# Performance work log

Measured on AMD Instinct MI355X. Metric: run time of the kernel, lower is better.

Reference implementation:

```python
import jax, jax.numpy as jnp
import numpy as np

G = 64          # voxel grid side
N_IN = 150000   # input points
N_OUT = 150000  # output points
K = 3           # cubic kernel size
CIN = 32
FOUT = 64


def _make_cloud(rng, n):
    flat = rng.permutation(G ** 3)[:n]
    x = flat % G
    y = (flat // G) % G
    z = flat // (G * G)
    pos = np.stack([x, y, z], axis=-1).astype(np.float32) + 0.5  # voxel centers
    return flat, pos


def setup_inputs() -> dict:
    rng = np.random.default_rng(0)
    flat_in, inp_pos = _make_cloud(rng, N_IN)
    _, out_pos = _make_cloud(np.random.default_rng(1), N_OUT)

    # Fixed-radius (Linf, r = K*voxel*0.51 = 1.53) search on the grid ==
    # 3x3x3 voxel neighborhood lookup. Build dense voxel -> point-index map.
    grid = np.full(G ** 3, -1, dtype=np.int64)
    grid[flat_in] = np.arange(N_IN)
    offs = np.stack(np.meshgrid(*([np.arange(-1, 2)] * 3), indexing='ij'), -1).reshape(-1, 3)  # [27,3]
    out_vox = (out_pos - 0.5).astype(np.int64)              # [M,3]
    nb = out_vox[:, None, :] + offs[None, :, :]             # [M,27,3]
    inb = ((nb >= 0) & (nb < G)).all(-1)                    # [M,27]
    flat = nb[..., 0] + G * nb[..., 1] + G * G * nb[..., 2]
    flat = np.where(inb, flat, 0)
    found = grid[flat]
    mask = inb & (found >= 0)
    nbr_idx = np.where(mask, found, 0).astype(np.int32)

    key = jax.random.key(0)
    k1, k2, k3, k4, k5 = jax.random.split(key, 5)
    return {
        'inp_features': jax.random.normal(k1, (N_IN, CIN), jnp.float32),
        'inp_positions': jnp.asarray(inp_pos),
        'out_positions': jnp.asarray(out_pos),
        'voxel_size': jnp.asarray(1.0, jnp.float32),
        'inp_importance': jax.random.uniform(k2, (N_IN,), jnp.float32),
        'kernel': jax.random.uniform(k3, (K, K, K, CIN, FOUT), jnp.float32, -0.05, 0.05),
        'bias': jnp.zeros((FOUT,), jnp.float32) + 0.01 * jax.random.normal(k4, (FOUT,)),
        'neighbor_index': jnp.asarray(nbr_idx),
        'neighbor_mask': jnp.asarray(mask),
    }


def _sparse_conv(inp_features, inp_positions, out_positions, voxel_size,
                 inp_importance, kernel, bias, neighbor_index, neighbor_mask):
    # offset = 0 (odd kernel). extent = kernel_size * voxel_size.
    extent = K * voxel_size
    nbr_pos = inp_positions[neighbor_index]                  # [M,Kn,3]
    rel = nbr_pos - out_positions[:, None, :]                # [M,Kn,3]
    # identity coordinate mapping: normalize to [-1,1] over the extent
    n = 2.0 * rel / extent
    # align_corners=False mapping to filter coords, + offset (=0)
    fcoord = (n * 0.5 + 0.5) * K - 0.5                        # [M,Kn,3] (x,y,z)
    idx = jnp.clip(jnp.round(fcoord).astype(jnp.int32), 0, K - 1)
    # kernel is indexed [z,y,x,cin,cout]; positions are [x,y,z]
    flat_cell = idx[..., 2] * (K * K) + idx[..., 1] * K + idx[..., 0]   # [M,Kn]
    onehot = jax.nn.one_hot(flat_cell, K ** 3, dtype=inp_features.dtype)  # [M,Kn,27]
    w = (inp_importance[neighbor_index] * neighbor_mask.astype(inp_features.dtype))  # [M,Kn]
    feat = inp_features[neighbor_index] * w[..., None]       # [M,Kn,Cin]
    # accumulate neighbor features into their kernel cell, then contract with kernel
    cellfeat = jnp.einsum('mko,mkc->moc', onehot, feat)      # [M,27,Cin]
    wflat = kernel.reshape(K ** 3, CIN, FOUT)
    out = jnp.einsum('moc,ocf->mf', cellfeat, wflat)         # [M,F]
    return out + bias


def reference(inp_features, inp_positions, out_positions, voxel_size,
              inp_importance, kernel, bias, neighbor_index, neighbor_mask):
    return _sparse_conv(inp_features, inp_positions, out_positions, voxel_size,
                        inp_importance, kernel, bias, neighbor_index, neighbor_mask)
```

## Files before the change

### kernel.cpp

```cpp
#include <hip/hip_runtime.h>
#include <hip/hip_bf16.h>

#define CELLS 27
#define CIN   32
#define FOUT  64
#define M_OUT 150000
#define N_INP 150000
#define GDIM  64
#define NVOX  (GDIM * GDIM * GDIM)

#define GFEAT_SHORTS (NVOX * CIN)
#define GFEAT_BYTES  (GFEAT_SHORTS * 2)
#define OUTMAP_BYTES (NVOX * 4)
#define WT2_SHORTS   (CELLS * 4 * 64 * 8)
#define WT2_BYTES    (WT2_SHORTS * 2)
#define DENSE_WS     ((size_t)GFEAT_BYTES + OUTMAP_BYTES + WT2_BYTES)

#define ZROW  N_INP
#define PPG   64
#define GROUPS ((M_OUT + PPG - 1) / PPG)
#define FB_ROWS  (N_INP + 1)
#define FB_BYTES (FB_ROWS * CIN * 2)

typedef __attribute__((ext_vector_type(4))) float f32x4;
typedef __attribute__((ext_vector_type(8))) short bf16x8;
typedef __attribute__((ext_vector_type(4))) int   i32x4;

__device__ __forceinline__ short f2bf(float x) {
    union { __hip_bfloat16 h; short s; } u;
    u.h = __float2bfloat16(x);
    return u.s;
}


__global__ __launch_bounds__(256) void clear_kernel(unsigned short* __restrict__ gfeat,
                                                    int* __restrict__ outmap) {
    int t = blockIdx.x * 256 + threadIdx.x;
    if (t < 1048576) {
        ((i32x4*)gfeat)[t] = (i32x4){0, 0, 0, 0};
    } else {
        int u = t - 1048576;
        if (u < 65536) ((i32x4*)outmap)[u] = (i32x4){-1, -1, -1, -1};
    }
}

__global__ __launch_bounds__(256) void build_kernel(const float* __restrict__ feat,
                                                    const float* __restrict__ ipos,
                                                    const float* __restrict__ opos,
                                                    const float* __restrict__ imp,
                                                    const float* __restrict__ W,
                                                    unsigned short* __restrict__ gfeat,
                                                    int* __restrict__ outmap,
                                                    unsigned short* __restrict__ Wt2) {
    int t = blockIdx.x * 256 + threadIdx.x;
    if (t < N_INP * 4) {
        int p = t >> 2, c = t & 3;
        int x = (int)ipos[p * 3 + 0];
        int y = (int)ipos[p * 3 + 1];
        int z = (int)ipos[p * 3 + 2];
        int flat = x + (y << 6) + (z << 12);
        float wv = imp[p];
        const float* fp = feat + (size_t)p * CIN + c * 8;
        f32x4 f0 = *(const f32x4*)fp;
        f32x4 f1 = *(const f32x4*)(fp + 4);
        bf16x8 o;
        o[0] = f2bf(f0.x * wv); o[1] = f2bf(f0.y * wv);
        o[2] = f2bf(f0.z * wv); o[3] = f2bf(f0.w * wv);
        o[4] = f2bf(f1.x * wv); o[5] = f2bf(f1.y * wv);
        o[6] = f2bf(f1.z * wv); o[7] = f2bf(f1.w * wv);
        *(bf16x8*)(gfeat + (size_t)flat * CIN + c * 8) = o;
    } else if (t < N_INP * 4 + M_OUT) {
        int m = t - N_INP * 4;
        int x = (int)opos[m * 3 + 0];
        int y = (int)opos[m * 3 + 1];
        int z = (int)opos[m * 3 + 2];
        outmap[x + (y << 6) + (z << 12)] = m;
    } else {
        int v = t - (N_INP * 4 + M_OUT);
        if (v < CELLS * 4 * 64) {
            int l    = v & 63;
            int ct   = v >> 6;
            int tt   = ct & 3;
            int cell = ct >> 2;
            int fout = tt * 16 + (l & 15);
            int cin0 = (l >> 4) * 8;
            bf16x8 o;
#pragma unroll
            for (int j = 0; j < 8; ++j)
                o[j] = f2bf(W[cell * 2048 + (cin0 + j) * 64 + fout]);
            *(bf16x8*)(Wt2 + (size_t)v * 8) = o;
        }
    }
}

__global__ __launch_bounds__(256, 2) void conv_dense_kernel(
        const unsigned short* __restrict__ gfeat,
        const int*   __restrict__ outmap,
        const unsigned short* __restrict__ Wt2,
        const float* __restrict__ bias,
        float* __restrict__ out) {
    __shared__ __align__(16) unsigned char sh[48000];

    const int tid = threadIdx.x;
    const int bid = blockIdx.x;
    const int bx0 = (bid & 7) * 8;
    const int by0 = ((bid >> 3) & 7) * 8;
    const int bz0 = (bid >> 6) * 4;

#pragma unroll
    for (int it = 0; it < 10; ++it) {
        int c = it * 256 + tid;
        if (c < 2400) {
            int v = c >> 2, ch = c & 3;
            int q10  = (v * 6554) >> 16;
            int hx   = v - q10 * 10;
            int q100 = (q10 * 6554) >> 16;
            int hy   = q10 - q100 * 10;
            int hz   = q100;
            int gx = bx0 - 1 + hx, gy = by0 - 1 + hy, gz = bz0 - 1 + hz;
            bf16x8 val = {0, 0, 0, 0, 0, 0, 0, 0};
            if (((unsigned)gx < 64u) & ((unsigned)gy < 64u) & ((unsigned)gz < 64u)) {
                int flat = gx + (gy << 6) + (gz << 12);
                val = *(const bf16x8*)(gfeat + (size_t)flat * CIN + ch * 8);
            }
            *(bf16x8*)&sh[v * 80 + ch * 16] = val;
        }
    }
    __syncthreads();

    const int w    = tid >> 6;
    const int lane = tid & 63;
    const int r = lane & 15;
    const int g = lane >> 4;

    const unsigned char* Ab = sh + (r & 7) * 80 + (r >> 3) * 800 + w * 8000 + g * 16;
    const unsigned short* Bp = Wt2 + lane * 8;

    f32x4 acc[4][4];
#pragma unroll
    for (int mt = 0; mt < 4; ++mt)
#pragma unroll
        for (int nt = 0; nt < 4; ++nt) acc[mt][nt] = (f32x4){0.f, 0.f, 0.f, 0.f};

    bf16x8 bb[2][4];
#pragma unroll
    for (int nt = 0; nt < 4; ++nt)
        bb[0][nt] = *(const bf16x8*)(Bp + nt * 512);

#pragma unroll
    for (int cell = 0; cell < CELLS; ++cell) {
        const int cur = cell & 1, nxt = cur ^ 1;
        const int hx = cell % 3, hy = (cell / 3) % 3, hz = cell / 9;
        if (cell + 1 < CELLS) {
#pragma unroll
            for (int nt = 0; nt < 4; ++nt)
                bb[nxt][nt] = *(const bf16x8*)(Bp + (cell + 1) * 2048 + nt * 512);
        }
#pragma unroll
        for (int mt = 0; mt < 4; ++mt) {
            bf16x8 a = *(const bf16x8*)(Ab + hz * 8000 + (hy + 2 * mt) * 800 + hx * 80);
#pragma unroll
            for (int nt = 0; nt < 4; ++nt)
                acc[mt][nt] = __builtin_amdgcn_mfma_f32_16x16x32_bf16(a, bb[cur][nt],
                                                                      acc[mt][nt], 0, 0, 0);
        }
    }

    float bv0 = bias[r], bv1 = bias[16 + r], bv2 = bias[32 + r], bv3 = bias[48 + r];
    const int obase = bx0 + (by0 << 6) + ((bz0 + w) << 12);
#pragma unroll
    for (int mt = 0; mt < 4; ++mt) {
#pragma unroll
        for (int j = 0; j < 4; ++j) {
            int row = mt * 16 + g * 4 + j;
            int om = outmap[obase + (row & 7) + ((row >> 3) << 6)];
            if (om >= 0) {
                float* op = out + (size_t)om * FOUT + r;
                op[0]  = acc[mt][0][j] + bv0;
                op[16] = acc[mt][1][j] + bv1;
                op[32] = acc[mt][2][j] + bv2;
                op[48] = acc[mt][3][j] + bv3;
            }
        }
    }
}


#define CELL_OF(k) (((k) % 3) * 9 + (((k) / 3) % 3) * 3 + ((k) / 9))

__global__ __launch_bounds__(256) void prep_fb_kernel(const float* __restrict__ W,
                                                      const float* __restrict__ feat,
                                                      const float* __restrict__ imp,
                                                      unsigned short* __restrict__ Wt2,
                                                      unsigned short* __restrict__ fb) {
    int t = blockIdx.x * 256 + threadIdx.x;
    if (t < FB_ROWS * 4) {
        int i = t >> 2, c = t & 3;
        bf16x8 o = {0, 0, 0, 0, 0, 0, 0, 0};
        if (i < N_INP) {
            float w = imp[i];
            const float* fp = feat + (size_t)i * CIN + c * 8;
            f32x4 f0 = *(const f32x4*)fp;
            f32x4 f1 = *(const f32x4*)(fp + 4);
            o[0] = f2bf(f0.x * w); o[1] = f2bf(f0.y * w);
            o[2] = f2bf(f0.z * w); o[3] = f2bf(f0.w * w);
            o[4] = f2bf(f1.x * w); o[5] = f2bf(f1.y * w);
            o[6] = f2bf(f1.z * w); o[7] = f2bf(f1.w * w);
        }
        *(bf16x8*)(fb + (size_t)i * CIN + c * 8) = o;
    } else {
        int v = t - FB_ROWS * 4;
        if (v < CELLS * 4 * 64) {
            int l    = v & 63;
            int ct   = v >> 6;
            int tt   = ct & 3;
            int cell = ct >> 2;
            int fout = tt * 16 + (l & 15);
            int cin0 = (l >> 4) * 8;
            bf16x8 o;
#pragma unroll
            for (int j = 0; j < 8; ++j)
                o[j] = f2bf(W[cell * 2048 + (cin0 + j) * 64 + fout]);
            *(bf16x8*)(Wt2 + (size_t)v * 8) = o;
        }
    }
}

__global__ __launch_bounds__(128, 4) void conv64_kernel(
        const float* __restrict__ opos,
        const float* __restrict__ ipos,
        const int*   __restrict__ nbr,
        const unsigned short* __restrict__ Wt2,
        const unsigned short* __restrict__ fb,
        const float* __restrict__ bias,
        float* __restrict__ out) {
    __shared__ int s_idx[PPG][28];
    __shared__ int s_vox[PPG];
    __shared__ __align__(16) unsigned char s_A[2][4 * 1056];

    const int tid   = threadIdx.x;
    const int lane  = tid & 63;
    const int fhalf = tid >> 6;
    const int m0    = blockIdx.x * PPG;

    const int vx0 = (int)ipos[0];
    const int vy0 = (int)ipos[1];
    const int vz0 = (int)ipos[2];

    if (fhalf == 0) {
        int m = m0 + lane;
        int vp = -1;
        if (m < M_OUT) {
            vp = ((int)opos[m * 3 + 0] + 1) |
                 (((int)opos[m * 3 + 1] + 1) << 8) |
                 (((int)opos[m * 3 + 2] + 1) << 16);
        }
        s_vox[lane] = vp;
    }
    __syncthreads();

#pragma unroll
    for (int it = 0; it < 14; ++it) {
        int e = it * 128 + tid;
        if (e < CELLS * PPG) {
            int p = e / CELLS;
            int k = e - p * CELLS;
            int m = m0 + p;
            int id = (m < M_OUT) ? nbr[m * CELLS + k] : 0;
            int ox = k / 9, oy = (k / 3) % 3, oz = k % 3;
            int tgt = (vx0 - ox + 2) | ((vy0 - oy + 2) << 8) | ((vz0 - oz + 2) << 16);
            bool valid = (id != 0) | (s_vox[p] == tgt);
            s_idx[p][k] = valid ? id : ZROW;
        }
    }
    __syncthreads();

    const int st_c  = lane & 3;
    const int st_r0 = fhalf * 32 + (lane >> 2);
    const int st_r1 = st_r0 + 16;
    const unsigned short* fb_c = fb + st_c * 8;

    const int g = lane >> 4;
    const int r = lane & 15;
    const int wbase = fhalf * 2;

    {
        int i0 = s_idx[st_r0][0];
        int i1 = s_idx[st_r1][0];
        bf16x8 v0 = *(const bf16x8*)(fb_c + (size_t)i0 * CIN);
        bf16x8 v1 = *(const bf16x8*)(fb_c + (size_t)i1 * CIN);
        *(bf16x8*)&s_A[0][st_c * 1056 + st_r0 * 16] = v0;
        *(bf16x8*)&s_A[0][st_c * 1056 + st_r1 * 16] = v1;
    }
    bf16x8 cb0 = *(const bf16x8*)(Wt2 + (CELL_OF(0) * 4 + wbase + 0) * 512 + lane * 8);
    bf16x8 cb1 = *(const bf16x8*)(Wt2 + (CELL_OF(0) * 4 + wbase + 1) * 512 + lane * 8);
    __syncthreads();

    f32x4 acc[8];
#pragma unroll
    for (int i = 0; i < 8; ++i) acc[i] = (f32x4){0.f, 0.f, 0.f, 0.f};

#pragma unroll
    for (int k = 0; k < CELLS; ++k) {
        const int b = k & 1;
        bf16x8 v0, v1, nb0, nb1;
        const bool more = (k + 1 < CELLS);
        if (more) {
            int i0 = s_idx[st_r0][k + 1];
            int i1 = s_idx[st_r1][k + 1];
            v0 = *(const bf16x8*)(fb_c + (size_t)i0 * CIN);
            v1 = *(const bf16x8*)(fb_c + (size_t)i1 * CIN);
            const int c2 = CELL_OF(k + 1);
            nb0 = *(const bf16x8*)(Wt2 + (c2 * 4 + wbase + 0) * 512 + lane * 8);
            nb1 = *(const bf16x8*)(Wt2 + (c2 * 4 + wbase + 1) * 512 + lane * 8);
        }
        const unsigned char* Ab = &s_A[b][0];
        bf16x8 a0 = *(const bf16x8*)(Ab + g * 1056 +   0 + r * 16);
        bf16x8 a1 = *(const bf16x8*)(Ab + g * 1056 + 256 + r * 16);
        bf16x8 a2 = *(const bf16x8*)(Ab + g * 1056 + 512 + r * 16);
        bf16x8 a3 = *(const bf16x8*)(Ab + g * 1056 + 768 + r * 16);
        acc[0] = __builtin_amdgcn_mfma_f32_16x16x32_bf16(a0, cb0, acc[0], 0, 0, 0);
        acc[1] = __builtin_amdgcn_mfma_f32_16x16x32_bf16(a0, cb1, acc[1], 0, 0, 0);
        acc[2] = __builtin_amdgcn_mfma_f32_16x16x32_bf16(a1, cb0, acc[2], 0, 0, 0);
        acc[3] = __builtin_amdgcn_mfma_f32_16x16x32_bf16(a1, cb1, acc[3], 0, 0, 0);
        acc[4] = __builtin_amdgcn_mfma_f32_16x16x32_bf16(a2, cb0, acc[4], 0, 0, 0);
        acc[5] = __builtin_amdgcn_mfma_f32_16x16x32_bf16(a2, cb1, acc[5], 0, 0, 0);
        acc[6] = __builtin_amdgcn_mfma_f32_16x16x32_bf16(a3, cb0, acc[6], 0, 0, 0);
        acc[7] = __builtin_amdgcn_mfma_f32_16x16x32_bf16(a3, cb1, acc[7], 0, 0, 0);
        if (more) {
            *(bf16x8*)&s_A[b ^ 1][st_c * 1056 + st_r0 * 16] = v0;
            *(bf16x8*)&s_A[b ^ 1][st_c * 1056 + st_r1 * 16] = v1;
            cb0 = nb0;
            cb1 = nb1;
        }
        __syncthreads();
    }

    float bb0 = bias[fhalf * 32 + r];
    float bb1 = bias[fhalf * 32 + 16 + r];
#pragma unroll
    for (int h = 0; h < 4; ++h) {
        int base = m0 + h * 16 + 4 * g;
#pragma unroll
        for (int j = 0; j < 4; ++j) {
            int m = base + j;
            if (m < M_OUT) {
                float* op = out + (size_t)m * FOUT + fhalf * 32 + r;
                op[0]  = acc[h * 2 + 0][j] + bb0;
                op[16] = acc[h * 2 + 1][j] + bb1;
            }
        }
    }
}


extern "C" void kernel_launch(void* const* d_in, const int* in_sizes, int n_in,
                              void* d_out, int out_size, void* d_ws, size_t ws_size,
                              hipStream_t stream) {
    const float* feat = (const float*)d_in[0];
    const float* ipos = (const float*)d_in[1];
    const float* opos = (const float*)d_in[2];
    const float* imp  = (const float*)d_in[4];
    const float* W    = (const float*)d_in[5];
    const float* bias = (const float*)d_in[6];
    const int*   nbr  = (const int*)d_in[7];
    float* out = (float*)d_out;

    if (ws_size >= DENSE_WS) {
        unsigned short* gfeat = (unsigned short*)d_ws;
        int* outmap = (int*)((char*)d_ws + GFEAT_BYTES);
        unsigned short* Wt2 = (unsigned short*)((char*)d_ws + GFEAT_BYTES + OUTMAP_BYTES);

        hipLaunchKernelGGL(clear_kernel, dim3((1048576 + 65536 + 255) / 256), dim3(256),
                           0, stream, gfeat, outmap);
        int build_threads = N_INP * 4 + M_OUT + CELLS * 4 * 64;
        hipLaunchKernelGGL(build_kernel, dim3((build_threads + 255) / 256), dim3(256),
                           0, stream, feat, ipos, opos, imp, W, gfeat, outmap, Wt2);
        hipLaunchKernelGGL(conv_dense_kernel, dim3(1024), dim3(256), 0, stream,
                           gfeat, outmap, Wt2, bias, out);
    } else {
        unsigned short* Wt2 = (unsigned short*)d_ws;
        unsigned short* fb  = (unsigned short*)((char*)d_ws + WT2_BYTES);
        int prep_threads = FB_ROWS * 4 + CELLS * 4 * 64;
        hipLaunchKernelGGL(prep_fb_kernel, dim3((prep_threads + 255) / 256), dim3(256),
                           0, stream, W, feat, imp, Wt2, fb);
        hipLaunchKernelGGL(conv64_kernel, dim3(GROUPS), dim3(128), 0, stream,
                           opos, ipos, nbr, Wt2, fb, bias, out);
    }
}
```

Before: 149.0 us.

## Enlarge dense conv tile to 8x8x8 with channel-split LDS halo layout

The dense conv kernel now processes an 8x8x8 voxel block per 512-thread workgroup instead of 8x8x4 per 256 threads. The halo fraction drops from 10x10x6 to 10x10x10 per tile, so less gfeat is reloaded across neighbouring tiles. The LDS halo is stored channel-chunk-major (4 planes of 16-byte entries) rather than 80-byte padded voxels, and all global loads are issued before any LDS stores. The custom clear kernel is replaced by two hipMemsetAsync calls. The trade-off is fewer workgroups (512) and larger LDS per block, which may lower occupancy and load balance.

New measurement: 156.9 us. +5.3%, slower.

```diff
diff --git a/kernel.cpp b/kernel.cpp
--- a/kernel.cpp
+++ b/kernel.cpp
@@ -16,6 +16,9 @@
 #define WT2_BYTES    (WT2_SHORTS * 2)
 #define DENSE_WS     ((size_t)GFEAT_BYTES + OUTMAP_BYTES + WT2_BYTES)
 
+#define CHB   16032
+#define LDSSZ (4 * CHB)
+
 #define ZROW  N_INP
 #define PPG   64
 #define GROUPS ((M_OUT + PPG - 1) / PPG)
@@ -24,7 +27,6 @@
 
 typedef __attribute__((ext_vector_type(4))) float f32x4;
 typedef __attribute__((ext_vector_type(8))) short bf16x8;
-typedef __attribute__((ext_vector_type(4))) int   i32x4;
 
 __device__ __forceinline__ short f2bf(float x) {
     union { __hip_bfloat16 h; short s; } u;
@@ -32,17 +34,6 @@
     return u.s;
 }
 
-
-__global__ __launch_bounds__(256) void clear_kernel(unsigned short* __restrict__ gfeat,
-                                                    int* __restrict__ outmap) {
-    int t = blockIdx.x * 256 + threadIdx.x;
-    if (t < 1048576) {
-        ((i32x4*)gfeat)[t] = (i32x4){0, 0, 0, 0};
-    } else {
-        int u = t - 1048576;
-        if (u < 65536) ((i32x4*)outmap)[u] = (i32x4){-1, -1, -1, -1};
-    }
-}
 
 __global__ __launch_bounds__(256) void build_kernel(const float* __restrict__ feat,
                                                     const float* __restrict__ ipos,
@@ -93,24 +84,26 @@
     }
 }
 
-__global__ __launch_bounds__(256, 2) void conv_dense_kernel(
+__global__ __launch_bounds__(512, 4) void conv_dense8_kernel(
         const unsigned short* __restrict__ gfeat,
         const int*   __restrict__ outmap,
         const unsigned short* __restrict__ Wt2,
         const float* __restrict__ bias,
         float* __restrict__ out) {
-    __shared__ __align__(16) unsigned char sh[48000];
+    __shared__ __align__(16) unsigned char sh[LDSSZ];
 
     const int tid = threadIdx.x;
     const int bid = blockIdx.x;
     const int bx0 = (bid & 7) * 8;
     const int by0 = ((bid >> 3) & 7) * 8;
-    const int bz0 = (bid >> 6) * 4;
-
-#pragma unroll
-    for (int it = 0; it < 10; ++it) {
-        int c = it * 256 + tid;
-        if (c < 2400) {
+    const int bz0 = (bid >> 6) * 8;
+
+    bf16x8 hv[8];
+#pragma unroll
+    for (int it = 0; it < 8; ++it) {
+        int c = it * 512 + tid;
+        bf16x8 val = {0, 0, 0, 0, 0, 0, 0, 0};
+        if (c < 4000) {
             int v = c >> 2, ch = c & 3;
             int q10  = (v * 6554) >> 16;
             int hx   = v - q10 * 10;
@@ -118,12 +111,19 @@
             int hy   = q10 - q100 * 10;
             int hz   = q100;
             int gx = bx0 - 1 + hx, gy = by0 - 1 + hy, gz = bz0 - 1 + hz;
-            bf16x8 val = {0, 0, 0, 0, 0, 0, 0, 0};
             if (((unsigned)gx < 64u) & ((unsigned)gy < 64u) & ((unsigned)gz < 64u)) {
                 int flat = gx + (gy << 6) + (gz << 12);
                 val = *(const bf16x8*)(gfeat + (size_t)flat * CIN + ch * 8);
             }
-            *(bf16x8*)&sh[v * 80 + ch * 16] = val;
+        }
+        hv[it] = val;
+    }
+#pragma unroll
+    for (int it = 0; it < 8; ++it) {
+        int c = it * 512 + tid;
+        if (c < 4000) {
+            int v = c >> 2, ch = c & 3;
+            *(bf16x8*)&sh[ch * CHB + v * 16] = hv[it];
         }
     }
     __syncthreads();
@@ -133,7 +133,7 @@
     const int r = lane & 15;
     const int g = lane >> 4;
 
-    const unsigned char* Ab = sh + (r & 7) * 80 + (r >> 3) * 800 + w * 8000 + g * 16;
+    const unsigned char* Ab = sh + g * CHB + ((r & 7) + (r >> 3) * 10 + w * 100) * 16;
     const unsigned short* Bp = Wt2 + lane * 8;
 
     f32x4 acc[4][4];
@@ -150,7 +150,7 @@
 #pragma unroll
     for (int cell = 0; cell < CELLS; ++cell) {
         const int cur = cell & 1, nxt = cur ^ 1;
-        const int hx = cell % 3, hy = (cell / 3) % 3, hz = cell / 9;
+        const int cx = cell % 3, cy = (cell / 3) % 3, cz = cell / 9;
         if (cell + 1 < CELLS) {
 #pragma unroll
             for (int nt = 0; nt < 4; ++nt)
@@ -158,7 +158,7 @@
         }
 #pragma unroll
         for (int mt = 0; mt < 4; ++mt) {
-            bf16x8 a = *(const bf16x8*)(Ab + hz * 8000 + (hy + 2 * mt) * 800 + hx * 80);
+            bf16x8 a = *(const bf16x8*)(Ab + (cx + (cy + 2 * mt) * 10 + cz * 100) * 16);
 #pragma unroll
             for (int nt = 0; nt < 4; ++nt)
                 acc[mt][nt] = __builtin_amdgcn_mfma_f32_16x16x32_bf16(a, bb[cur][nt],
@@ -167,13 +167,13 @@
     }
 
     float bv0 = bias[r], bv1 = bias[16 + r], bv2 = bias[32 + r], bv3 = bias[48 + r];
-    const int obase = bx0 + (by0 << 6) + ((bz0 + w) << 12);
 #pragma unroll
     for (int mt = 0; mt < 4; ++mt) {
 #pragma unroll
         for (int j = 0; j < 4; ++j) {
-            int row = mt * 16 + g * 4 + j;
-            int om = outmap[obase + (row & 7) + ((row >> 3) << 6)];
+            int p  = mt * 16 + g * 4 + j;
+            int px = p & 7, py = p >> 3;
+            int om = outmap[(bx0 + px) + ((by0 + py) << 6) + ((bz0 + w) << 12)];
             if (om >= 0) {
                 float* op = out + (size_t)om * FOUT + r;
                 op[0]  = acc[mt][0][j] + bv0;
@@ -371,12 +371,12 @@
         int* outmap = (int*)((char*)d_ws + GFEAT_BYTES);
         unsigned short* Wt2 = (unsigned short*)((char*)d_ws + GFEAT_BYTES + OUTMAP_BYTES);
 
-        hipLaunchKernelGGL(clear_kernel, dim3((1048576 + 65536 + 255) / 256), dim3(256),
-                           0, stream, gfeat, outmap);
+        hipMemsetAsync(gfeat, 0x00, GFEAT_BYTES, stream);
+        hipMemsetAsync(outmap, 0xFF, OUTMAP_BYTES, stream);
         int build_threads = N_INP * 4 + M_OUT + CELLS * 4 * 64;
         hipLaunchKernelGGL(build_kernel, dim3((build_threads + 255) / 256), dim3(256),
                            0, stream, feat, ipos, opos, imp, W, gfeat, outmap, Wt2);
-        hipLaunchKernelGGL(conv_dense_kernel, dim3(1024), dim3(256), 0, stream,
+        hipLaunchKernelGGL(conv_dense8_kernel, dim3(512), dim3(512), 0, stream,
                            gfeat, outmap, Wt2, bias, out);
     } else {
         unsigned short* Wt2 = (unsigned short*)d_ws;
```
